# Performance work log

Hardware: AMD Instinct MI355X
Metric: run time of the kernel (lower is better)

The kernel has to match this reference:

```python
import jax, jax.numpy as jnp
import numpy as np

B, NG, GS, D, L, NDL = 16, 50, 20, 256, 3, 2
N = NG * GS  # 1000


def setup_inputs() -> dict:
    key = jax.random.key(0)
    ks = jax.random.split(key, 8)
    amino_embd = jax.random.normal(ks[0], (B, NG, GS, D), dtype=jnp.float32)
    c = (jax.random.uniform(ks[1], (B, N, N)) < 0.02).astype(jnp.float32)
    prot_contacts = jnp.clip(c + jnp.transpose(c, (0, 2, 1)), 0.0, 1.0)
    # small init for bilinear W (original: random_uniform ~ +/-0.05) keeps exp() stable
    W_list = 0.01 * jax.random.normal(ks[2], (L, D, D), dtype=jnp.float32)
    dense_W = jax.random.normal(ks[3], (L, NDL, D, D), dtype=jnp.float32) / np.sqrt(D)
    dense_b = jnp.zeros((L, NDL, D), dtype=jnp.float32)
    final_W = jax.random.normal(ks[4], (D, D), dtype=jnp.float32) / np.sqrt(D)
    final_b = jnp.zeros((D,), dtype=jnp.float32)
    return {"amino_embd": amino_embd, "prot_contacts": prot_contacts,
            "W_list": W_list, "dense_W": dense_W, "dense_b": dense_b,
            "final_W": final_W, "final_b": final_b}


def reference(amino_embd, prot_contacts, W_list, dense_W, dense_b, final_W, final_b):
    dt = amino_embd.dtype
    eye = jnp.eye(N, dtype=dt)
    A = prot_contacts + eye  # contact map with self loops, [B,N,N]
    x = amino_embd.reshape(B, N, D)
    for l in range(L):
        x0 = x
        # bilinear non-local scores: [B,N,N]
        scores = jnp.einsum('bid,de,bje->bij', x0, W_list[l], x0)
        s = jnp.exp(scores) + jnp.asarray(1e-5, dt) * eye
        s = s * A                                   # mask by contacts + self loop
        s = s / jnp.sum(s, axis=-1, keepdims=True)  # row-normalize
        x = jnp.einsum('bij,bjd->bid', s, x0)       # aggregate
        for dl in range(NDL):
            x = jax.nn.relu(x @ dense_W[l, dl] + dense_b[l, dl])
        x = x + x0  # skip connection
    x = x @ final_W + final_b
    return x.reshape(B, NG, GS, D)
```

## Files before the change

### kernel.cpp

```cpp
#include <hip/hip_runtime.h>

#define BB 16
#define NN 1000
#define DD 256
#define LL 3
#define MAXNZ 256
#define MROWS (BB * NN)

typedef _Float16 f16x8 __attribute__((ext_vector_type(8)));
typedef float f32x4 __attribute__((ext_vector_type(4)));

union H8 { _Float16 h[8]; int4 v; };

__device__ __forceinline__ float dot4(float4 a, float4 b) {
    return fmaf(a.x, b.x, fmaf(a.y, b.y, fmaf(a.z, b.z, a.w * b.w)));
}
__device__ __forceinline__ void fma4(float4& a, float w, float4 v) {
    a.x = fmaf(w, v.x, a.x); a.y = fmaf(w, v.y, a.y);
    a.z = fmaf(w, v.z, a.z); a.w = fmaf(w, v.w, a.w);
}

__global__ __launch_bounds__(256) void convert_w(
    const float* __restrict__ W_list, const float* __restrict__ dense_W,
    const float* __restrict__ final_W,
    _Float16* __restrict__ wt_hi, _Float16* __restrict__ wt_lo)
{
    __shared__ float T[64][68];
    int blk = blockIdx.x;
    int mat = blk >> 4;
    int tile = blk & 15;
    int tk = (tile >> 2) * 64, tn = (tile & 3) * 64;
    const float* src = (mat < 3) ? (W_list + (size_t)mat * 65536)
                     : (mat < 9) ? (dense_W + (size_t)(mat - 3) * 65536)
                                 : final_W;
    int t = threadIdx.x;
    {
        int k = t >> 2, nc = (t & 3) * 16;
        const float* sp = src + (size_t)(tk + k) * 256 + tn + nc;
        float4 v0 = *(const float4*)(sp + 0);
        float4 v1 = *(const float4*)(sp + 4);
        float4 v2 = *(const float4*)(sp + 8);
        float4 v3 = *(const float4*)(sp + 12);
        *(float4*)&T[k][nc + 0]  = v0;
        *(float4*)&T[k][nc + 4]  = v1;
        *(float4*)&T[k][nc + 8]  = v2;
        *(float4*)&T[k][nc + 12] = v3;
    }
    __syncthreads();
    int n = t >> 2, kc = (t & 3) * 16;
    H8 hh0, hh1, ll0, ll1;
    #pragma unroll
    for (int i = 0; i < 16; ++i) {
        float x = T[kc + i][n];
        _Float16 hi = (_Float16)x;
        float r = x - (float)hi;
        _Float16 lo = (_Float16)(r * 2048.0f);
        if (i < 8) { hh0.h[i] = hi; ll0.h[i] = lo; }
        else       { hh1.h[i - 8] = hi; ll1.h[i - 8] = lo; }
    }
    size_t o = (size_t)mat * 65536 + (size_t)(tn + n) * 256 + tk + kc;
    *(int4*)(wt_hi + o)     = hh0.v;
    *(int4*)(wt_hi + o + 8) = hh1.v;
    *(int4*)(wt_lo + o)     = ll0.v;
    *(int4*)(wt_lo + o + 8) = ll1.v;
}

__global__ __launch_bounds__(256) void build_sparse(
    const float* __restrict__ contacts,
    int* __restrict__ idx, int* __restrict__ cnt, float* __restrict__ adiag)
{
    int wave = (int)((blockIdx.x * blockDim.x + threadIdx.x) >> 6);
    int lane = threadIdx.x & 63;
    if (wave >= MROWS) return;
    int b = wave / NN;
    int i = wave - b * NN;
    const float* row = contacts + (size_t)b * NN * NN + (size_t)i * NN;
    int* out = idx + (size_t)wave * MAXNZ;
    int count = 0;
    for (int j0 = 0; j0 < NN; j0 += 64) {
        int j = j0 + lane;
        float v = (j < NN) ? row[j] : 0.0f;
        bool p = (v != 0.0f) && (j != i);
        unsigned long long bal = __ballot(p);
        if (p) {
            int pre = __popcll(bal & ((1ull << lane) - 1ull));
            out[count + pre] = j;
        }
        count += __popcll(bal);
    }
    if (lane == 0) {
        cnt[wave] = count;
        adiag[wave] = row[i] + 1.0f;
    }
}

__global__ __launch_bounds__(256) void sparse_agg(
    const float* __restrict__ y, const float* __restrict__ x0,
    const int* __restrict__ idx, const int* __restrict__ cnt,
    const float* __restrict__ adiag, float* __restrict__ xout)
{
    int bid = blockIdx.x;
    int xcd = bid & 7;
    int chunk = bid >> 3;
    int row = xcd * 2000 + chunk * 4 + (int)(threadIdx.x >> 6);
    row = __builtin_amdgcn_readfirstlane(row);
    int lane = threadIdx.x & 63;
    int g = lane >> 4, s = lane & 15;
    int b = row / NN;

    const float* yp = y + (size_t)row * DD + s * 4;
    float4 y0 = *(const float4*)(yp +   0);
    float4 y1 = *(const float4*)(yp +  64);
    float4 y2 = *(const float4*)(yp + 128);
    float4 y3 = *(const float4*)(yp + 192);
    const float* xip = x0 + (size_t)row * DD + s * 4;
    float4 xi0 = *(const float4*)(xip +   0);
    float4 xi1 = *(const float4*)(xip +  64);
    float4 xi2 = *(const float4*)(xip + 128);
    float4 xi3 = *(const float4*)(xip + 192);
    const float* xb = x0 + (size_t)b * NN * DD;

    float p = dot4(y0, xi0) + dot4(y1, xi1) + dot4(y2, xi2) + dot4(y3, xi3);
    p += __shfl_xor(p, 1); p += __shfl_xor(p, 2);
    p += __shfl_xor(p, 4); p += __shfl_xor(p, 8);
    float wd = (g == 0) ? (__expf(p) + 1e-5f) * adiag[row] : 0.0f;
    float denom = wd;
    float4 a0 = make_float4(0.f, 0.f, 0.f, 0.f), a1 = a0, a2 = a0, a3 = a0;
    fma4(a0, wd, xi0); fma4(a1, wd, xi1); fma4(a2, wd, xi2); fma4(a3, wd, xi3);

    const int c = cnt[row];
    const int* ip = idx + (size_t)row * MAXNZ;
    const int iters = (c + 3) >> 2;

    int j0 = (g < c) ? ip[g] : 0;
    int j1 = (4 + g < c) ? ip[4 + g] : 0;
    bool vok = g < c;
    const float* xjp = xb + (size_t)j0 * DD + s * 4;
    float4 v0 = *(const float4*)(xjp +   0);
    float4 v1 = *(const float4*)(xjp +  64);
    float4 v2 = *(const float4*)(xjp + 128);
    float4 v3 = *(const float4*)(xjp + 192);

    for (int t = 0; t < iters; ++t) {
        int k2 = (t + 2) * 4 + g;
        int j2 = (k2 < c) ? ip[k2] : 0;
        const float* np = xb + (size_t)j1 * DD + s * 4;
        float4 n0 = *(const float4*)(np +   0);
        float4 n1 = *(const float4*)(np +  64);
        float4 n2 = *(const float4*)(np + 128);
        float4 n3 = *(const float4*)(np + 192);

        float q = dot4(y0, v0) + dot4(y1, v1) + dot4(y2, v2) + dot4(y3, v3);
        q += __shfl_xor(q, 1); q += __shfl_xor(q, 2);
        q += __shfl_xor(q, 4); q += __shfl_xor(q, 8);
        float w = vok ? __expf(q) : 0.0f;
        denom += w;
        fma4(a0, w, v0); fma4(a1, w, v1); fma4(a2, w, v2); fma4(a3, w, v3);

        v0 = n0; v1 = n1; v2 = n2; v3 = n3;
        j1 = j2;
        vok = (t + 1) * 4 + g < c;
    }

#define XG(x) x += __shfl_xor(x, 16); x += __shfl_xor(x, 32);
    XG(denom);
    XG(a0.x) XG(a0.y) XG(a0.z) XG(a0.w)
    XG(a1.x) XG(a1.y) XG(a1.z) XG(a1.w)
    XG(a2.x) XG(a2.y) XG(a2.z) XG(a2.w)
    XG(a3.x) XG(a3.y) XG(a3.z) XG(a3.w)
#undef XG

    float inv = 1.0f / denom;
    float4 o = (g == 0) ? a0 : (g == 1) ? a1 : (g == 2) ? a2 : a3;
    o.x *= inv; o.y *= inv; o.z *= inv; o.w *= inv;
    *(float4*)(xout + (size_t)row * DD + g * 64 + s * 4) = o;
}

__global__ __launch_bounds__(256, 4) void gemm16(
    const float* __restrict__ A,
    const _Float16* __restrict__ wt_hi, const _Float16* __restrict__ wt_lo,
    const float* __restrict__ bias, const float* __restrict__ skip,
    float* __restrict__ C, int relu)
{
    __shared__ __align__(16) char smem[32768];
    char* Ah = smem;
    char* Al = smem + 8192;
    char* Bh = smem + 16384;
    char* Bl = smem + 24576;

    int tid = threadIdx.x;
    int mBase = blockIdx.y * 64;
    int nBase = blockIdx.x * 64;

    int sm = tid >> 2;
    int kc = (tid & 3) * 16;
    const float*    Ag  = A     + (size_t)(mBase + sm) * 256 + kc;
    const _Float16* Bgh = wt_hi + (size_t)(nBase + sm) * 256 + kc;
    const _Float16* Bgl = wt_lo + (size_t)(nBase + sm) * 256 + kc;
    int sbase = sm * 128 + kc * 2;
    int swz = (sm & 7) << 4;

    int l = tid & 63;
    int wv = tid >> 6;
    int wm = (wv >> 1) * 32, wn = (wv & 1) * 32;
    int lr = l & 15;
    int lkb = (l >> 4) * 16;

    f32x4 acc0[2][2] = {};
    f32x4 acc1[2][2] = {};

    for (int kb = 0; kb < 256; kb += 64) {
        float4 f0 = *(const float4*)(Ag + kb + 0);
        float4 f1 = *(const float4*)(Ag + kb + 4);
        float4 f2 = *(const float4*)(Ag + kb + 8);
        float4 f3 = *(const float4*)(Ag + kb + 12);
        int4 gh0 = *(const int4*)(Bgh + kb);
        int4 gh1 = *(const int4*)(Bgh + kb + 8);
        int4 gl0 = *(const int4*)(Bgl + kb);
        int4 gl1 = *(const int4*)(Bgl + kb + 8);

        float xs[16] = {f0.x, f0.y, f0.z, f0.w, f1.x, f1.y, f1.z, f1.w,
                        f2.x, f2.y, f2.z, f2.w, f3.x, f3.y, f3.z, f3.w};
        H8 ah0, ah1, al0, al1;
        #pragma unroll
        for (int i = 0; i < 16; ++i) {
            float x = xs[i];
            _Float16 hi = (_Float16)x;
            float r = x - (float)hi;
            _Float16 lo = (_Float16)(r * 2048.0f);
            if (i < 8) { ah0.h[i] = hi; al0.h[i] = lo; }
            else       { ah1.h[i - 8] = hi; al1.h[i - 8] = lo; }
        }

        __syncthreads();
        *(int4*)(Ah + ((sbase +  0) ^ swz)) = ah0.v;
        *(int4*)(Ah + ((sbase + 16) ^ swz)) = ah1.v;
        *(int4*)(Al + ((sbase +  0) ^ swz)) = al0.v;
        *(int4*)(Al + ((sbase + 16) ^ swz)) = al1.v;
        *(int4*)(Bh + ((sbase +  0) ^ swz)) = gh0;
        *(int4*)(Bh + ((sbase + 16) ^ swz)) = gh1;
        *(int4*)(Bl + ((sbase +  0) ^ swz)) = gl0;
        *(int4*)(Bl + ((sbase + 16) ^ swz)) = gl1;
        __syncthreads();

        #pragma unroll
        for (int kk = 0; kk < 2; ++kk) {
            int kby = kk * 64 + lkb;
            f16x8 fah[2], fal[2], fbh[2], fbl[2];
            #pragma unroll
            for (int mt = 0; mt < 2; ++mt) {
                int ml = wm + mt * 16 + lr;
                int off = (ml * 128 + kby) ^ ((ml & 7) << 4);
                fah[mt] = *(const f16x8*)(Ah + off);
                fal[mt] = *(const f16x8*)(Al + off);
            }
            #pragma unroll
            for (int nt = 0; nt < 2; ++nt) {
                int nl = wn + nt * 16 + lr;
                int off = (nl * 128 + kby) ^ ((nl & 7) << 4);
                fbh[nt] = *(const f16x8*)(Bh + off);
                fbl[nt] = *(const f16x8*)(Bl + off);
            }
            #pragma unroll
            for (int mt = 0; mt < 2; ++mt)
                #pragma unroll
                for (int nt = 0; nt < 2; ++nt) {
                    acc0[mt][nt] = __builtin_amdgcn_mfma_f32_16x16x32_f16(
                        fah[mt], fbh[nt], acc0[mt][nt], 0, 0, 0);
                    acc1[mt][nt] = __builtin_amdgcn_mfma_f32_16x16x32_f16(
                        fah[mt], fbl[nt], acc1[mt][nt], 0, 0, 0);
                    acc1[mt][nt] = __builtin_amdgcn_mfma_f32_16x16x32_f16(
                        fal[mt], fbh[nt], acc1[mt][nt], 0, 0, 0);
                }
        }
    }

    #pragma unroll
    for (int mt = 0; mt < 2; ++mt) {
        #pragma unroll
        for (int nt = 0; nt < 2; ++nt) {
            int n = nBase + wn + nt * 16 + lr;
            float bval = bias ? bias[n] : 0.0f;
            #pragma unroll
            for (int q = 0; q < 4; ++q) {
                int m = mBase + wm + mt * 16 + (l >> 4) * 4 + q;
                float v = acc0[mt][nt][q] + acc1[mt][nt][q] * 4.8828125e-4f + bval;
                if (relu) v = fmaxf(v, 0.0f);
                if (skip) v += skip[(size_t)m * 256 + n];
                C[(size_t)m * 256 + n] = v;
            }
        }
    }
}

extern "C" void kernel_launch(void* const* d_in, const int* in_sizes, int n_in,
                              void* d_out, int out_size, void* d_ws, size_t ws_size,
                              hipStream_t stream)
{
    const float* x_in     = (const float*)d_in[0];
    const float* contacts = (const float*)d_in[1];
    const float* W_list   = (const float*)d_in[2];
    const float* dense_W  = (const float*)d_in[3];
    const float* dense_b  = (const float*)d_in[4];
    const float* final_W  = (const float*)d_in[5];
    const float* final_b  = (const float*)d_in[6];
    float* out = (float*)d_out;

    char* ws = (char*)d_ws;
    const size_t bufBytes = (size_t)MROWS * DD * sizeof(float);
    float* bufA = (float*)(ws);
    float* bufB = (float*)(ws + bufBytes);
    float* bufC = (float*)(ws + 2 * bufBytes);
    int*   idx  = (int*)(ws + 3 * bufBytes);
    int*   cnt  = (int*)(ws + 3 * bufBytes + (size_t)MROWS * MAXNZ * sizeof(int));
    float* adiag = (float*)((char*)cnt + (size_t)MROWS * sizeof(int));
    _Float16* wt_hi = (_Float16*)((char*)adiag + (size_t)MROWS * sizeof(float));
    _Float16* wt_lo = wt_hi + (size_t)10 * 65536;

    convert_w<<<160, 256, 0, stream>>>(W_list, dense_W, final_W, wt_hi, wt_lo);
    build_sparse<<<MROWS / 4, 256, 0, stream>>>(contacts, idx, cnt, adiag);

    dim3 gg(DD / 64, MROWS / 64);
    const float* curx = x_in;
    for (int l = 0; l < LL; ++l) {
        float* yv = bufA;
        float* ov = (l == 1) ? bufC : bufB;
        gemm16<<<gg, 256, 0, stream>>>(curx, wt_hi + (size_t)l * 65536,
                                       wt_lo + (size_t)l * 65536,
                                       nullptr, nullptr, yv, 0);
        sparse_agg<<<MROWS / 4, 256, 0, stream>>>(yv, curx, idx, cnt, adiag, ov);
        gemm16<<<gg, 256, 0, stream>>>(ov, wt_hi + (size_t)(3 + l * 2) * 65536,
                                       wt_lo + (size_t)(3 + l * 2) * 65536,
                                       dense_b + (size_t)(l * 2 + 0) * 256,
                                       nullptr, yv, 1);
        gemm16<<<gg, 256, 0, stream>>>(yv, wt_hi + (size_t)(4 + l * 2) * 65536,
                                       wt_lo + (size_t)(4 + l * 2) * 65536,
                                       dense_b + (size_t)(l * 2 + 1) * 256,
                                       curx, ov, 1);
        curx = ov;
    }
    gemm16<<<gg, 256, 0, stream>>>(curx, wt_hi + (size_t)9 * 65536,
                                   wt_lo + (size_t)9 * 65536,
                                   final_b, nullptr, out, 0);
}
```

Baseline: 297.4 us.

## Store activations as split fp16 hi/lo planes and widen GEMM N-tile

```diff
diff --git a/kernel.cpp b/kernel.cpp
--- a/kernel.cpp
+++ b/kernel.cpp
@@ -6,18 +6,27 @@
 #define LL 3
 #define MAXNZ 256
 #define MROWS (BB * NN)
+#define SPLIT_SCALE 2048.0f
+#define INV_SPLIT 4.8828125e-4f
 
 typedef _Float16 f16x8 __attribute__((ext_vector_type(8)));
+typedef _Float16 f16x2 __attribute__((ext_vector_type(2)));
 typedef float f32x4 __attribute__((ext_vector_type(4)));
 
-union H8 { _Float16 h[8]; int4 v; };
-
-__device__ __forceinline__ float dot4(float4 a, float4 b) {
-    return fmaf(a.x, b.x, fmaf(a.y, b.y, fmaf(a.z, b.z, a.w * b.w)));
-}
-__device__ __forceinline__ void fma4(float4& a, float w, float4 v) {
-    a.x = fmaf(w, v.x, a.x); a.y = fmaf(w, v.y, a.y);
-    a.z = fmaf(w, v.z, a.z); a.w = fmaf(w, v.w, a.w);
+union H8 { f16x8 v; f16x2 p[4]; _Float16 h[8]; int4 i4; };
+
+#if defined(__has_builtin)
+#if __has_builtin(__builtin_amdgcn_fdot2)
+#define HAS_FDOT2 1
+#endif
+#endif
+
+__device__ __forceinline__ float dot2f(f16x2 a, f16x2 b, float c) {
+#ifdef HAS_FDOT2
+    return __builtin_amdgcn_fdot2(a, b, c, false);
+#else
+    return fmaf((float)a[0], (float)b[0], fmaf((float)a[1], (float)b[1], c));
+#endif
 }
 
 __global__ __launch_bounds__(256) void convert_w(
@@ -37,14 +46,10 @@
     {
         int k = t >> 2, nc = (t & 3) * 16;
         const float* sp = src + (size_t)(tk + k) * 256 + tn + nc;
-        float4 v0 = *(const float4*)(sp + 0);
-        float4 v1 = *(const float4*)(sp + 4);
-        float4 v2 = *(const float4*)(sp + 8);
-        float4 v3 = *(const float4*)(sp + 12);
-        *(float4*)&T[k][nc + 0]  = v0;
-        *(float4*)&T[k][nc + 4]  = v1;
-        *(float4*)&T[k][nc + 8]  = v2;
-        *(float4*)&T[k][nc + 12] = v3;
+        *(float4*)&T[k][nc + 0]  = *(const float4*)(sp + 0);
+        *(float4*)&T[k][nc + 4]  = *(const float4*)(sp + 4);
+        *(float4*)&T[k][nc + 8]  = *(const float4*)(sp + 8);
+        *(float4*)&T[k][nc + 12] = *(const float4*)(sp + 12);
     }
     __syncthreads();
     int n = t >> 2, kc = (t & 3) * 16;
@@ -53,16 +58,35 @@
     for (int i = 0; i < 16; ++i) {
         float x = T[kc + i][n];
         _Float16 hi = (_Float16)x;
-        float r = x - (float)hi;
-        _Float16 lo = (_Float16)(r * 2048.0f);
+        _Float16 lo = (_Float16)((x - (float)hi) * SPLIT_SCALE);
         if (i < 8) { hh0.h[i] = hi; ll0.h[i] = lo; }
         else       { hh1.h[i - 8] = hi; ll1.h[i - 8] = lo; }
     }
     size_t o = (size_t)mat * 65536 + (size_t)(tn + n) * 256 + tk + kc;
-    *(int4*)(wt_hi + o)     = hh0.v;
-    *(int4*)(wt_hi + o + 8) = hh1.v;
-    *(int4*)(wt_lo + o)     = ll0.v;
-    *(int4*)(wt_lo + o + 8) = ll1.v;
+    *(int4*)(wt_hi + o)     = hh0.i4;
+    *(int4*)(wt_hi + o + 8) = hh1.i4;
+    *(int4*)(wt_lo + o)     = ll0.i4;
+    *(int4*)(wt_lo + o + 8) = ll1.i4;
+}
+
+__global__ __launch_bounds__(256) void convert_x(
+    const float* __restrict__ in, _Float16* __restrict__ hi,
+    _Float16* __restrict__ lo)
+{
+    size_t gid = (size_t)blockIdx.x * 256 + threadIdx.x;
+    const float* p = in + gid * 8;
+    float4 a = *(const float4*)p;
+    float4 b = *(const float4*)(p + 4);
+    float xs[8] = {a.x, a.y, a.z, a.w, b.x, b.y, b.z, b.w};
+    H8 hh, ll;
+    #pragma unroll
+    for (int i = 0; i < 8; ++i) {
+        _Float16 h = (_Float16)xs[i];
+        hh.h[i] = h;
+        ll.h[i] = (_Float16)((xs[i] - (float)h) * SPLIT_SCALE);
+    }
+    *(int4*)(hi + gid * 8) = hh.i4;
+    *(int4*)(lo + gid * 8) = ll.i4;
 }
 
 __global__ __launch_bounds__(256) void build_sparse(
@@ -95,9 +119,11 @@
 }
 
 __global__ __launch_bounds__(256) void sparse_agg(
-    const float* __restrict__ y, const float* __restrict__ x0,
+    const _Float16* __restrict__ yhi,
+    const _Float16* __restrict__ xhi, const _Float16* __restrict__ xlo,
     const int* __restrict__ idx, const int* __restrict__ cnt,
-    const float* __restrict__ adiag, float* __restrict__ xout)
+    const float* __restrict__ adiag,
+    _Float16* __restrict__ ohi, _Float16* __restrict__ olo)
 {
     int bid = blockIdx.x;
     int xcd = bid & 7;
@@ -108,25 +134,37 @@
     int g = lane >> 4, s = lane & 15;
     int b = row / NN;
 
-    const float* yp = y + (size_t)row * DD + s * 4;
-    float4 y0 = *(const float4*)(yp +   0);
-    float4 y1 = *(const float4*)(yp +  64);
-    float4 y2 = *(const float4*)(yp + 128);
-    float4 y3 = *(const float4*)(yp + 192);
-    const float* xip = x0 + (size_t)row * DD + s * 4;
-    float4 xi0 = *(const float4*)(xip +   0);
-    float4 xi1 = *(const float4*)(xip +  64);
-    float4 xi2 = *(const float4*)(xip + 128);
-    float4 xi3 = *(const float4*)(xip + 192);
-    const float* xb = x0 + (size_t)b * NN * DD;
-
-    float p = dot4(y0, xi0) + dot4(y1, xi1) + dot4(y2, xi2) + dot4(y3, xi3);
+    const _Float16* yp = yhi + (size_t)row * DD + s * 8;
+    H8 yh0, yh1;
+    yh0.i4 = *(const int4*)yp;
+    yh1.i4 = *(const int4*)(yp + 128);
+
+    const _Float16* xph = xhi + (size_t)row * DD + s * 8;
+    const _Float16* xpl = xlo + (size_t)row * DD + s * 8;
+    H8 xih0, xih1, xil0, xil1;
+    xih0.i4 = *(const int4*)xph;       xih1.i4 = *(const int4*)(xph + 128);
+    xil0.i4 = *(const int4*)xpl;       xil1.i4 = *(const int4*)(xpl + 128);
+    float xi[16];
+    #pragma unroll
+    for (int u = 0; u < 8; ++u) {
+        xi[u]     = fmaf((float)xil0.h[u], INV_SPLIT, (float)xih0.h[u]);
+        xi[8 + u] = fmaf((float)xil1.h[u], INV_SPLIT, (float)xih1.h[u]);
+    }
+    const _Float16* xb = xhi + (size_t)b * NN * DD;
+
+    float p = 0.0f;
+    #pragma unroll
+    for (int u = 0; u < 8; ++u) {
+        p = fmaf((float)yh0.h[u], xi[u], p);
+        p = fmaf((float)yh1.h[u], xi[8 + u], p);
+    }
     p += __shfl_xor(p, 1); p += __shfl_xor(p, 2);
     p += __shfl_xor(p, 4); p += __shfl_xor(p, 8);
     float wd = (g == 0) ? (__expf(p) + 1e-5f) * adiag[row] : 0.0f;
     float denom = wd;
-    float4 a0 = make_float4(0.f, 0.f, 0.f, 0.f), a1 = a0, a2 = a0, a3 = a0;
-    fma4(a0, wd, xi0); fma4(a1, wd, xi1); fma4(a2, wd, xi2); fma4(a3, wd, xi3);
+    float acc[16];
+    #pragma unroll
+    for (int u = 0; u < 16; ++u) acc[u] = wd * xi[u];
 
     const int c = cnt[row];
     const int* ip = idx + (size_t)row * MAXNZ;
@@ -135,118 +173,127 @@
     int j0 = (g < c) ? ip[g] : 0;
     int j1 = (4 + g < c) ? ip[4 + g] : 0;
     bool vok = g < c;
-    const float* xjp = xb + (size_t)j0 * DD + s * 4;
-    float4 v0 = *(const float4*)(xjp +   0);
-    float4 v1 = *(const float4*)(xjp +  64);
-    float4 v2 = *(const float4*)(xjp + 128);
-    float4 v3 = *(const float4*)(xjp + 192);
+    H8 v0, v1;
+    {
+        const _Float16* xp = xb + (size_t)j0 * DD + s * 8;
+        v0.i4 = *(const int4*)xp;
+        v1.i4 = *(const int4*)(xp + 128);
+    }
 
     for (int t = 0; t < iters; ++t) {
         int k2 = (t + 2) * 4 + g;
         int j2 = (k2 < c) ? ip[k2] : 0;
-        const float* np = xb + (size_t)j1 * DD + s * 4;
-        float4 n0 = *(const float4*)(np +   0);
-        float4 n1 = *(const float4*)(np +  64);
-        float4 n2 = *(const float4*)(np + 128);
-        float4 n3 = *(const float4*)(np + 192);
-
-        float q = dot4(y0, v0) + dot4(y1, v1) + dot4(y2, v2) + dot4(y3, v3);
+        H8 n0, n1;
+        const _Float16* np = xb + (size_t)j1 * DD + s * 8;
+        n0.i4 = *(const int4*)np;
+        n1.i4 = *(const int4*)(np + 128);
+
+        float q = 0.0f;
+        #pragma unroll
+        for (int i = 0; i < 4; ++i) q = dot2f(yh0.p[i], v0.p[i], q);
+        #pragma unroll
+        for (int i = 0; i < 4; ++i) q = dot2f(yh1.p[i], v1.p[i], q);
         q += __shfl_xor(q, 1); q += __shfl_xor(q, 2);
         q += __shfl_xor(q, 4); q += __shfl_xor(q, 8);
         float w = vok ? __expf(q) : 0.0f;
         denom += w;
-        fma4(a0, w, v0); fma4(a1, w, v1); fma4(a2, w, v2); fma4(a3, w, v3);
-
-        v0 = n0; v1 = n1; v2 = n2; v3 = n3;
+        #pragma unroll
+        for (int u = 0; u < 8; ++u) {
+            acc[u]     = fmaf(w, (float)v0.h[u], acc[u]);
+            acc[8 + u] = fmaf(w, (float)v1.h[u], acc[8 + u]);
+        }
+
+        v0 = n0; v1 = n1;
         j1 = j2;
         vok = (t + 1) * 4 + g < c;
     }
 
 #define XG(x) x += __shfl_xor(x, 16); x += __shfl_xor(x, 32);
     XG(denom);
-    XG(a0.x) XG(a0.y) XG(a0.z) XG(a0.w)
-    XG(a1.x) XG(a1.y) XG(a1.z) XG(a1.w)
-    XG(a2.x) XG(a2.y) XG(a2.z) XG(a2.w)
-    XG(a3.x) XG(a3.y) XG(a3.z) XG(a3.w)
+    #pragma unroll
+    for (int u = 0; u < 16; ++u) { XG(acc[u]) }
 #undef XG
 
     float inv = 1.0f / denom;
-    float4 o = (g == 0) ? a0 : (g == 1) ? a1 : (g == 2) ? a2 : a3;
-    o.x *= inv; o.y *= inv; o.z *= inv; o.w *= inv;
-    *(float4*)(xout + (size_t)row * DD + g * 64 + s * 4) = o;
-}
-
-__global__ __launch_bounds__(256, 4) void gemm16(
-    const float* __restrict__ A,
-    const _Float16* __restrict__ wt_hi, const _Float16* __restrict__ wt_lo,
-    const float* __restrict__ bias, const float* __restrict__ skip,
-    float* __restrict__ C, int relu)
-{
-    __shared__ __align__(16) char smem[32768];
+    int half = (g & 1) * 8;
+    H8 st;
+    #pragma unroll
+    for (int i = 0; i < 8; ++i) {
+        float x = acc[half + i] * inv;
+        _Float16 h = (_Float16)x;
+        st.h[i] = (g & 2) ? (_Float16)((x - (float)h) * SPLIT_SCALE) : h;
+    }
+    _Float16* dst = ((g & 2) ? olo : ohi) + (size_t)row * DD + (g & 1) * 128 + s * 8;
+    *(int4*)dst = st.i4;
+}
+
+__global__ __launch_bounds__(256, 3) void gemm16(
+    const _Float16* __restrict__ Ahi, const _Float16* __restrict__ Alo,
+    const _Float16* __restrict__ Bhi, const _Float16* __restrict__ Blo,
+    const float* __restrict__ bias,
+    const _Float16* __restrict__ Shi, const _Float16* __restrict__ Slo,
+    _Float16* __restrict__ Chi, _Float16* __restrict__ Clo,
+    float* __restrict__ Cf32, int relu)
+{
+    __shared__ __align__(16) char smem[49152];
     char* Ah = smem;
     char* Al = smem + 8192;
     char* Bh = smem + 16384;
-    char* Bl = smem + 24576;
+    char* Bl = smem + 32768;
 
     int tid = threadIdx.x;
     int mBase = blockIdx.y * 64;
-    int nBase = blockIdx.x * 64;
-
-    int sm = tid >> 2;
-    int kc = (tid & 3) * 16;
-    const float*    Ag  = A     + (size_t)(mBase + sm) * 256 + kc;
-    const _Float16* Bgh = wt_hi + (size_t)(nBase + sm) * 256 + kc;
-    const _Float16* Bgl = wt_lo + (size_t)(nBase + sm) * 256 + kc;
-    int sbase = sm * 128 + kc * 2;
-    int swz = (sm & 7) << 4;
-
-    int l = tid & 63;
-    int wv = tid >> 6;
-    int wm = (wv >> 1) * 32, wn = (wv & 1) * 32;
-    int lr = l & 15;
-    int lkb = (l >> 4) * 16;
-
-    f32x4 acc0[2][2] = {};
-    f32x4 acc1[2][2] = {};
+    int nBase = blockIdx.x * 128;
+
+    int sm = tid >> 2, kc = (tid & 3) * 16;
+    int sb = tid >> 1, kcb = (tid & 1) * 32;
+    const _Float16* gAh = Ahi + (size_t)(mBase + sm) * 256 + kc;
+    const _Float16* gAl = Alo + (size_t)(mBase + sm) * 256 + kc;
+    const _Float16* gBh = Bhi + (size_t)(nBase + sb) * 256 + kcb;
+    const _Float16* gBl = Blo + (size_t)(nBase + sb) * 256 + kcb;
+    int sbA = sm * 128 + kc * 2, swzA = (sm & 7) << 4;
+    int sbB = sb * 128 + kcb * 2, swzB = (sb & 7) << 4;
+
+    int l = tid & 63, wv = tid >> 6;
+    int wm = (wv & 1) * 32, wn = (wv >> 1) * 64;
+    int lr = l & 15, lkb = (l >> 4) * 16;
+
+    f32x4 acc0[2][4] = {};
+    f32x4 acc1[2][4] = {};
 
     for (int kb = 0; kb < 256; kb += 64) {
-        float4 f0 = *(const float4*)(Ag + kb + 0);
-        float4 f1 = *(const float4*)(Ag + kb + 4);
-        float4 f2 = *(const float4*)(Ag + kb + 8);
-        float4 f3 = *(const float4*)(Ag + kb + 12);
-        int4 gh0 = *(const int4*)(Bgh + kb);
-        int4 gh1 = *(const int4*)(Bgh + kb + 8);
-        int4 gl0 = *(const int4*)(Bgl + kb);
-        int4 gl1 = *(const int4*)(Bgl + kb + 8);
-
-        float xs[16] = {f0.x, f0.y, f0.z, f0.w, f1.x, f1.y, f1.z, f1.w,
-                        f2.x, f2.y, f2.z, f2.w, f3.x, f3.y, f3.z, f3.w};
-        H8 ah0, ah1, al0, al1;
-        #pragma unroll
-        for (int i = 0; i < 16; ++i) {
-            float x = xs[i];
-            _Float16 hi = (_Float16)x;
-            float r = x - (float)hi;
-            _Float16 lo = (_Float16)(r * 2048.0f);
-            if (i < 8) { ah0.h[i] = hi; al0.h[i] = lo; }
-            else       { ah1.h[i - 8] = hi; al1.h[i - 8] = lo; }
-        }
+        int4 ah0 = *(const int4*)(gAh + kb);
+        int4 ah1 = *(const int4*)(gAh + kb + 8);
+        int4 al0 = *(const int4*)(gAl + kb);
+        int4 al1 = *(const int4*)(gAl + kb + 8);
+        int4 bh0 = *(const int4*)(gBh + kb);
+        int4 bh1 = *(const int4*)(gBh + kb + 8);
+        int4 bh2 = *(const int4*)(gBh + kb + 16);
+        int4 bh3 = *(const int4*)(gBh + kb + 24);
+        int4 bl0 = *(const int4*)(gBl + kb);
+        int4 bl1 = *(const int4*)(gBl + kb + 8);
+        int4 bl2 = *(const int4*)(gBl + kb + 16);
+        int4 bl3 = *(const int4*)(gBl + kb + 24);
 
         __syncthreads();
-        *(int4*)(Ah + ((sbase +  0) ^ swz)) = ah0.v;
-        *(int4*)(Ah + ((sbase + 16) ^ swz)) = ah1.v;
-        *(int4*)(Al + ((sbase +  0) ^ swz)) = al0.v;
-        *(int4*)(Al + ((sbase + 16) ^ swz)) = al1.v;
-        *(int4*)(Bh + ((sbase +  0) ^ swz)) = gh0;
-        *(int4*)(Bh + ((sbase + 16) ^ swz)) = gh1;
-        *(int4*)(Bl + ((sbase +  0) ^ swz)) = gl0;
-        *(int4*)(Bl + ((sbase + 16) ^ swz)) = gl1;
+        *(int4*)(Ah + ((sbA +  0) ^ swzA)) = ah0;
+        *(int4*)(Ah + ((sbA + 16) ^ swzA)) = ah1;
+        *(int4*)(Al + ((sbA +  0) ^ swzA)) = al0;
+        *(int4*)(Al + ((sbA + 16) ^ swzA)) = al1;
+        *(int4*)(Bh + ((sbB +  0) ^ swzB)) = bh0;
+        *(int4*)(Bh + ((sbB + 16) ^ swzB)) = bh1;
+        *(int4*)(Bh + ((sbB + 32) ^ swzB)) = bh2;
+        *(int4*)(Bh + ((sbB + 48) ^ swzB)) = bh3;
+        *(int4*)(Bl + ((sbB +  0) ^ swzB)) = bl0;
+        *(int4*)(Bl + ((sbB + 16) ^ swzB)) = bl1;
+        *(int4*)(Bl + ((sbB + 32) ^ swzB)) = bl2;
+        *(int4*)(Bl + ((sbB + 48) ^ swzB)) = bl3;
         __syncthreads();
 
         #pragma unroll
         for (int kk = 0; kk < 2; ++kk) {
             int kby = kk * 64 + lkb;
-            f16x8 fah[2], fal[2], fbh[2], fbl[2];
+            f16x8 fah[2], fal[2];
             #pragma unroll
             for (int mt = 0; mt < 2; ++mt) {
                 int ml = wm + mt * 16 + lr;
@@ -254,8 +301,9 @@
                 fah[mt] = *(const f16x8*)(Ah + off);
                 fal[mt] = *(const f16x8*)(Al + off);
             }
+            f16x8 fbh[4], fbl[4];
             #pragma unroll
-            for (int nt = 0; nt < 2; ++nt) {
+            for (int nt = 0; nt < 4; ++nt) {
                 int nl = wn + nt * 16 + lr;
                 int off = (nl * 128 + kby) ^ ((nl & 7) << 4);
                 fbh[nt] = *(const f16x8*)(Bh + off);
@@ -264,7 +312,7 @@
             #pragma unroll
             for (int mt = 0; mt < 2; ++mt)
                 #pragma unroll
-                for (int nt = 0; nt < 2; ++nt) {
+                for (int nt = 0; nt < 4; ++nt) {
                     acc0[mt][nt] = __builtin_amdgcn_mfma_f32_16x16x32_f16(
                         fah[mt], fbh[nt], acc0[mt][nt], 0, 0, 0);
                     acc1[mt][nt] = __builtin_amdgcn_mfma_f32_16x16x32_f16(
@@ -278,16 +326,23 @@
     #pragma unroll
     for (int mt = 0; mt < 2; ++mt) {
         #pragma unroll
-        for (int nt = 0; nt < 2; ++nt) {
+        for (int nt = 0; nt < 4; ++nt) {
             int n = nBase + wn + nt * 16 + lr;
-            float bval = bias ? bias[n] : 0.0f;
+            float bv = bias ? bias[n] : 0.0f;
             #pragma unroll
             for (int q = 0; q < 4; ++q) {
                 int m = mBase + wm + mt * 16 + (l >> 4) * 4 + q;
-                float v = acc0[mt][nt][q] + acc1[mt][nt][q] * 4.8828125e-4f + bval;
+                size_t o = (size_t)m * 256 + n;
+                float v = acc0[mt][nt][q] + acc1[mt][nt][q] * INV_SPLIT + bv;
                 if (relu) v = fmaxf(v, 0.0f);
-                if (skip) v += skip[(size_t)m * 256 + n];
-                C[(size_t)m * 256 + n] = v;
+                if (Shi) v += (float)Shi[o] + (float)Slo[o] * INV_SPLIT;
+                if (Cf32) {
+                    Cf32[o] = v;
+                } else {
+                    _Float16 h = (_Float16)v;
+                    Chi[o] = h;
+                    Clo[o] = (_Float16)((v - (float)h) * SPLIT_SCALE);
+                }
             }
         }
     }
@@ -307,39 +362,52 @@
     float* out = (float*)d_out;
 
     char* ws = (char*)d_ws;
-    const size_t bufBytes = (size_t)MROWS * DD * sizeof(float);
-    float* bufA = (float*)(ws);
-    float* bufB = (float*)(ws + bufBytes);
-    float* bufC = (float*)(ws + 2 * bufBytes);
-    int*   idx  = (int*)(ws + 3 * bufBytes);
-    int*   cnt  = (int*)(ws + 3 * bufBytes + (size_t)MROWS * MAXNZ * sizeof(int));
+    const size_t PL = (size_t)MROWS * DD;
+    _Float16* pl[8];
+    for (int i = 0; i < 8; ++i) pl[i] = (_Float16*)ws + (size_t)i * PL;
+    char* p8 = ws + 8 * PL * sizeof(_Float16);
+    int*   idx   = (int*)p8;
+    int*   cnt   = (int*)(p8 + (size_t)MROWS * MAXNZ * sizeof(int));
     float* adiag = (float*)((char*)cnt + (size_t)MROWS * sizeof(int));
     _Float16* wt_hi = (_Float16*)((char*)adiag + (size_t)MROWS * sizeof(float));
     _Float16* wt_lo = wt_hi + (size_t)10 * 65536;
 
     convert_w<<<160, 256, 0, stream>>>(W_list, dense_W, final_W, wt_hi, wt_lo);
+    convert_x<<<MROWS * DD / (256 * 8), 256, 0, stream>>>(x_in, pl[0], pl[1]);
     build_sparse<<<MROWS / 4, 256, 0, stream>>>(contacts, idx, cnt, adiag);
 
-    dim3 gg(DD / 64, MROWS / 64);
-    const float* curx = x_in;
+    dim3 gg(2, MROWS / 64);
+    int cur = 0;
     for (int l = 0; l < LL; ++l) {
-        float* yv = bufA;
-        float* ov = (l == 1) ? bufC : bufB;
-        gemm16<<<gg, 256, 0, stream>>>(curx, wt_hi + (size_t)l * 65536,
+        int oth = 1 - cur;
+        _Float16 *x0h = pl[2 * cur], *x0l = pl[2 * cur + 1];
+        _Float16 *yh  = pl[2 * oth], *yl  = pl[2 * oth + 1];
+        _Float16 *xah = pl[4], *xal = pl[5];
+        _Float16 *xbh = pl[6], *xbl = pl[7];
+        gemm16<<<gg, 256, 0, stream>>>(x0h, x0l,
+                                       wt_hi + (size_t)l * 65536,
                                        wt_lo + (size_t)l * 65536,
-                                       nullptr, nullptr, yv, 0);
-        sparse_agg<<<MROWS / 4, 256, 0, stream>>>(yv, curx, idx, cnt, adiag, ov);
-        gemm16<<<gg, 256, 0, stream>>>(ov, wt_hi + (size_t)(3 + l * 2) * 65536,
+                                       nullptr, nullptr, nullptr,
+                                       yh, yl, nullptr, 0);
+        sparse_agg<<<MROWS / 4, 256, 0, stream>>>(yh, x0h, x0l, idx, cnt, adiag,
+                                                  xah, xal);
+        gemm16<<<gg, 256, 0, stream>>>(xah, xal,
+                                       wt_hi + (size_t)(3 + l * 2) * 65536,
                                        wt_lo + (size_t)(3 + l * 2) * 65536,
                                        dense_b + (size_t)(l * 2 + 0) * 256,
-                                       nullptr, yv, 1);
-        gemm16<<<gg, 256, 0, stream>>>(yv, wt_hi + (size_t)(4 + l * 2) * 65536,
+                                       nullptr, nullptr,
+                                       xbh, xbl, nullptr, 1);
+        gemm16<<<gg, 256, 0, stream>>>(xbh, xbl,
+                                       wt_hi + (size_t)(4 + l * 2) * 65536,
                                        wt_lo + (size_t)(4 + l * 2) * 65536,
                                        dense_b + (size_t)(l * 2 + 1) * 256,
-                                       curx, ov, 1);
-        curx = ov;
-    }
-    gemm16<<<gg, 256, 0, stream>>>(curx, wt_hi + (size_t)9 * 65536,
+                                       x0h, x0l,
+                                       yh, yl, nullptr, 1);
+        cur = oth;
+    }
+    gemm16<<<gg, 256, 0, stream>>>(pl[2 * cur], pl[2 * cur + 1],
+                                   wt_hi + (size_t)9 * 65536,
                                    wt_lo + (size_t)9 * 65536,
-                                   final_b, nullptr, out, 0);
-}
+                                   final_b, nullptr, nullptr,
+                                   nullptr, nullptr, out, 0);
+}
```

Measured after the change: 295.1 us. About the same (-0.8%).
